# Kernel optimization log

Measured on AMD Instinct MI355X. Metric: run time of the kernel, lower is better.

The kernel has to match this reference:

```python
import jax, jax.numpy as jnp
import numpy as np


def setup_inputs() -> dict:
    key = jax.random.key(0)
    k1, k2, k3 = jax.random.split(key, 3)
    B, N, D = 16, 2048, 128
    q = jax.random.normal(k1, (B, N, D), dtype=jnp.float32)
    k = jax.random.normal(k2, (B, D, N), dtype=jnp.float32)
    v = jax.random.normal(k3, (B, N, D), dtype=jnp.float32)
    return {"q": q, "k": k, "v": v}


def reference(q, k, v):
    # scores: [B, N, N] — note NO 1/sqrt(d) scaling, matching the source
    scores = jnp.einsum('bnd,bdm->bnm', q, k)
    probs = jax.nn.softmax(scores, axis=-1)
    out = jnp.einsum('bnm,bmd->bnd', probs, v)  # [B, N, D]
    return out
```

## Files before the change

kernel.cpp:

```cpp
#include <hip/hip_runtime.h>
#include <hip/hip_bf16.h>


typedef __attribute__((ext_vector_type(8))) _Float16 f16x8;
typedef __attribute__((ext_vector_type(4))) float f32x4;

constexpr int Bz = 16;
constexpr int Nn = 2048;
constexpr int Dd = 128;
constexpr int BM = 64;
constexpr int BN = 64;

__device__ __forceinline__ int swz(int r) { return (r ^ (r >> 3)) & 7; }
__device__ __forceinline__ int swzP(int row) { return (row >> 1) & 6; }

__device__ __forceinline__ uint packh2(float a, float b) {
    union { _Float16 h[2]; uint u; } p;
    p.h[0] = (_Float16)a; p.h[1] = (_Float16)b;
    return p.u;
}
__device__ __forceinline__ ushort f2h_bits(float a) {
    union { _Float16 h; ushort u; } p;
    p.h = (_Float16)a;
    return p.u;
}

template <int CTRL>
__device__ __forceinline__ float dpp_mov(float x) {
    int y = __builtin_amdgcn_mov_dpp(__builtin_bit_cast(int, x), CTRL, 0xF, 0xF, true);
    return __builtin_bit_cast(float, y);
}
template <typename Op>
__device__ __forceinline__ float allred16(float x, Op op) {
    x = op(x, dpp_mov<0xB1>(x));
    x = op(x, dpp_mov<0x4E>(x));
    x = op(x, dpp_mov<0x124>(x));
    x = op(x, dpp_mov<0x128>(x));
    return x;
}

__global__ __launch_bounds__(256, 2)
void fattn_kernel(const float* __restrict__ qg,
                  const float* __restrict__ kg,
                  const float* __restrict__ vg,
                  float* __restrict__ og)
{
    __shared__ ushort lds_k[BN * Dd];
    __shared__ ushort lds_v[Dd * BN];
    __shared__ ushort lds_p[4][16 * BN];
    uint* const lds_k32 = (uint*)lds_k;
    uint* const lds_v32 = (uint*)lds_v;

    const int bid  = blockIdx.x;
    const int xcd  = bid & 7;
    const int idx  = bid >> 3;
    const int b    = xcd * 2 + (idx >> 5);
    const int q0   = (idx & 31) * BM;
    const int tid  = threadIdx.x;
    const int wv   = tid >> 6;
    const int lane = tid & 63;
    const int quad = lane >> 4;
    const int l15  = lane & 15;

    f16x8 qf[4];
    {
        const float* qp = qg + (size_t)(b * Nn + q0 + wv * 16 + l15) * Dd + quad * 8;
        #pragma unroll
        for (int c = 0; c < 4; ++c) {
            float4 x0 = *(const float4*)(qp + c * 32);
            float4 x1 = *(const float4*)(qp + c * 32 + 4);
            const float xv[8] = {x0.x, x0.y, x0.z, x0.w, x1.x, x1.y, x1.z, x1.w};
            union { f16x8 v; _Float16 e[8]; } u;
            #pragma unroll
            for (int j = 0; j < 8; ++j) u.e[j] = (_Float16)xv[j];
            qf[c] = u.v;
        }
    }

    f32x4 accO[8];
    #pragma unroll
    for (int i = 0; i < 8; ++i) accO[i] = f32x4{0.f, 0.f, 0.f, 0.f};
    float m_i[4], l_i[4];
    #pragma unroll
    for (int r = 0; r < 4; ++r) { m_i[r] = -1e30f; l_i[r] = 0.f; }

    const int kgrp = tid & 7;
    const int krow = tid >> 3;
    const int vgrp = tid & 15;
    const int vrow = tid >> 4;

    const float* kbase = kg + (size_t)b * Dd * Nn;
    const float* vbase = vg + (size_t)b * Nn * Dd;

    float4 kr[8], vr[8];
    auto issue_loads = [&](int n0) {
        #pragma unroll
        for (int pass = 0; pass < 2; ++pass) {
            const int d0 = krow * 2 + pass * 64;
            const float* s0 = kbase + (size_t)d0 * Nn + n0 + kgrp * 8;
            kr[pass * 4 + 0] = ((const float4*)s0)[0];
            kr[pass * 4 + 1] = ((const float4*)s0)[1];
            kr[pass * 4 + 2] = ((const float4*)(s0 + Nn))[0];
            kr[pass * 4 + 3] = ((const float4*)(s0 + Nn))[1];
            const int kk0 = vrow * 2 + pass * 32;
            const float* t0 = vbase + (size_t)(n0 + kk0) * Dd + vgrp * 8;
            vr[pass * 4 + 0] = ((const float4*)t0)[0];
            vr[pass * 4 + 1] = ((const float4*)t0)[1];
            vr[pass * 4 + 2] = ((const float4*)(t0 + Dd))[0];
            vr[pass * 4 + 3] = ((const float4*)(t0 + Dd))[1];
        }
    };
    auto write_lds = [&]() {
        #pragma unroll
        for (int pass = 0; pass < 2; ++pass) {
            const int d0 = krow * 2 + pass * 64;
            const float* av = (const float*)&kr[pass * 4 + 0];
            const float* bv = (const float*)&kr[pass * 4 + 2];
            #pragma unroll
            for (int j = 0; j < 8; ++j) {
                const int n = kgrp * 8 + j;
                lds_k32[n * (Dd / 2) + ((d0 >> 1) ^ (swz(n) << 2))] = packh2(av[j], bv[j]);
            }
            const int kk0 = vrow * 2 + pass * 32;
            const float* cv = (const float*)&vr[pass * 4 + 0];
            const float* dv = (const float*)&vr[pass * 4 + 2];
            #pragma unroll
            for (int j = 0; j < 8; ++j) {
                const int dd = vgrp * 8 + j;
                lds_v32[dd * (BN / 2) + ((kk0 >> 1) ^ (swz(dd) << 2))] = packh2(cv[j], dv[j]);
            }
        }
    };

    issue_loads(0);

    for (int it = 0; it < Nn / BN; ++it) {
        write_lds();
        __syncthreads();

        issue_loads(((it + 1) & 31) * BN);

        f32x4 accS[4];
        #pragma unroll
        for (int kt = 0; kt < 4; ++kt) {
            f32x4 s = f32x4{0.f, 0.f, 0.f, 0.f};
            const int row = kt * 16 + l15;
            const int sw = swz(row) << 3;
            #pragma unroll
            for (int c = 0; c < 4; ++c) {
                f16x8 kf = *(const f16x8*)&lds_k[row * Dd + ((c * 32 + quad * 8) ^ sw)];
                s = __builtin_amdgcn_mfma_f32_16x16x32_f16(qf[c], kf, s, 0, 0, 0);
            }
            accS[kt] = s;
        }

        float alpha[4];
        #pragma unroll
        for (int r = 0; r < 4; ++r) {
            float t = fmaxf(fmaxf(accS[0][r], accS[1][r]), fmaxf(accS[2][r], accS[3][r]));
            t = allred16(t, [](float a, float bb) { return fmaxf(a, bb); });
            const float mn = fmaxf(m_i[r], t);
            alpha[r] = __expf(m_i[r] - mn);
            m_i[r] = mn;
        }
        #pragma unroll
        for (int r = 0; r < 4; ++r) {
            float local = 0.f;
            #pragma unroll
            for (int kt = 0; kt < 4; ++kt) {
                const float p = __expf(accS[kt][r] - m_i[r]);
                accS[kt][r] = p;
                local += p;
            }
            l_i[r] = l_i[r] * alpha[r] + local;
        }

        #pragma unroll
        for (int dt = 0; dt < 8; ++dt) {
            #pragma unroll
            for (int r = 0; r < 4; ++r)
                accO[dt][r] *= alpha[r];
        }

        ushort* pl = &lds_p[wv][0];
        #pragma unroll
        for (int kt = 0; kt < 4; ++kt) {
            #pragma unroll
            for (int r = 0; r < 4; ++r) {
                const int row = quad * 4 + r;
                const int col = kt * 16 + l15;
                pl[row * BN + (col ^ (swzP(row) << 3))] = f2h_bits(accS[kt][r]);
            }
        }
        f16x8 pf[2];
        {
            const int row = l15;
            const int sw = swzP(row) << 3;
            pf[0] = *(const f16x8*)&pl[row * BN + ((quad * 8) ^ sw)];
            pf[1] = *(const f16x8*)&pl[row * BN + ((32 + quad * 8) ^ sw)];
        }

        #pragma unroll
        for (int dt = 0; dt < 8; ++dt) {
            const int row = dt * 16 + l15;
            const int sw = swz(row) << 3;
            f16x8 vf0 = *(const f16x8*)&lds_v[row * BN + ((quad * 8) ^ sw)];
            f16x8 vf1 = *(const f16x8*)&lds_v[row * BN + ((32 + quad * 8) ^ sw)];
            accO[dt] = __builtin_amdgcn_mfma_f32_16x16x32_f16(pf[0], vf0, accO[dt], 0, 0, 0);
            accO[dt] = __builtin_amdgcn_mfma_f32_16x16x32_f16(pf[1], vf1, accO[dt], 0, 0, 0);
        }
        __syncthreads();
    }

    float inv[4];
    #pragma unroll
    for (int r = 0; r < 4; ++r) {
        const float l = allred16(l_i[r], [](float a, float bb) { return a + bb; });
        inv[r] = 1.f / l;
    }
    float* ob = og + (size_t)(b * Nn + q0 + wv * 16) * Dd;
    #pragma unroll
    for (int dt = 0; dt < 8; ++dt) {
        #pragma unroll
        for (int r = 0; r < 4; ++r) {
            const int row = quad * 4 + r;
            const int col = dt * 16 + l15;
            ob[(size_t)row * Dd + col] = accO[dt][r] * inv[r];
        }
    }
}

extern "C" void kernel_launch(void* const* d_in, const int* in_sizes, int n_in,
                              void* d_out, int out_size, void* d_ws, size_t ws_size,
                              hipStream_t stream) {
    const float* q = (const float*)d_in[0];
    const float* k = (const float*)d_in[1];
    const float* v = (const float*)d_in[2];
    float* o = (float*)d_out;
    (void)d_ws; (void)ws_size; (void)in_sizes; (void)n_in; (void)out_size;
    fattn_kernel<<<dim3(Bz * (Nn / BM)), dim3(256), 0, stream>>>(q, k, v, o);
}
```

Measured before the change: 158.6 us.

## Double query tile per block so each wave handles two 16-row strips

Each block now covers 128 query rows instead of 64, and each wave processes two 16-row sub-tiles that share every K/V fragment read from LDS. This halves the global K/V traffic and fp32-to-fp16 conversion per query row, and interleaves independent MFMA chains. In exchange, register pressure roughly doubles, so launch bounds drop to one block per CU. The grid also halves to 256 blocks, which is about one wave of blocks on the device and may hurt occupancy and latency hiding.

```diff
diff --git a/kernel.cpp b/kernel.cpp
--- a/kernel.cpp
+++ b/kernel.cpp
@@ -8,11 +8,11 @@
 constexpr int Bz = 16;
 constexpr int Nn = 2048;
 constexpr int Dd = 128;
-constexpr int BM = 64;
+constexpr int BM = 128;
 constexpr int BN = 64;
 
 __device__ __forceinline__ int swz(int r) { return (r ^ (r >> 3)) & 7; }
-__device__ __forceinline__ int swzP(int row) { return (row >> 1) & 6; }
+__device__ __forceinline__ int swzP2(int row) { return ((row >> 1) & 6) | (row & 1); }
 
 __device__ __forceinline__ uint packh2(float a, float b) {
     union { _Float16 h[2]; uint u; } p;
@@ -39,7 +39,7 @@
     return x;
 }
 
-__global__ __launch_bounds__(256, 2)
+__global__ __launch_bounds__(256, 1)
 void fattn_kernel(const float* __restrict__ qg,
                   const float* __restrict__ kg,
                   const float* __restrict__ vg,
@@ -47,24 +47,25 @@
 {
     __shared__ ushort lds_k[BN * Dd];
     __shared__ ushort lds_v[Dd * BN];
-    __shared__ ushort lds_p[4][16 * BN];
+    __shared__ ushort lds_p[4][32 * BN];
     uint* const lds_k32 = (uint*)lds_k;
     uint* const lds_v32 = (uint*)lds_v;
 
     const int bid  = blockIdx.x;
     const int xcd  = bid & 7;
     const int idx  = bid >> 3;
-    const int b    = xcd * 2 + (idx >> 5);
-    const int q0   = (idx & 31) * BM;
+    const int b    = xcd * 2 + (idx >> 4);
+    const int q0   = (idx & 15) * BM;
     const int tid  = threadIdx.x;
     const int wv   = tid >> 6;
     const int lane = tid & 63;
     const int quad = lane >> 4;
     const int l15  = lane & 15;
 
-    f16x8 qf[4];
-    {
-        const float* qp = qg + (size_t)(b * Nn + q0 + wv * 16 + l15) * Dd + quad * 8;
+    f16x8 qf[2][4];
+    #pragma unroll
+    for (int s = 0; s < 2; ++s) {
+        const float* qp = qg + (size_t)(b * Nn + q0 + wv * 32 + s * 16 + l15) * Dd + quad * 8;
         #pragma unroll
         for (int c = 0; c < 4; ++c) {
             float4 x0 = *(const float4*)(qp + c * 32);
@@ -73,16 +74,19 @@
             union { f16x8 v; _Float16 e[8]; } u;
             #pragma unroll
             for (int j = 0; j < 8; ++j) u.e[j] = (_Float16)xv[j];
-            qf[c] = u.v;
-        }
-    }
-
-    f32x4 accO[8];
+            qf[s][c] = u.v;
+        }
+    }
+
+    f32x4 accO[2][8];
+    float m_i[2][4], l_i[2][4];
     #pragma unroll
-    for (int i = 0; i < 8; ++i) accO[i] = f32x4{0.f, 0.f, 0.f, 0.f};
-    float m_i[4], l_i[4];
-    #pragma unroll
-    for (int r = 0; r < 4; ++r) { m_i[r] = -1e30f; l_i[r] = 0.f; }
+    for (int s = 0; s < 2; ++s) {
+        #pragma unroll
+        for (int i = 0; i < 8; ++i) accO[s][i] = f32x4{0.f, 0.f, 0.f, 0.f};
+        #pragma unroll
+        for (int r = 0; r < 4; ++r) { m_i[s][r] = -1e30f; l_i[s][r] = 0.f; }
+    }
 
     const int kgrp = tid & 7;
     const int krow = tid >> 3;
@@ -140,64 +144,74 @@
 
         issue_loads(((it + 1) & 31) * BN);
 
-        f32x4 accS[4];
+        f32x4 accS[2][4];
         #pragma unroll
         for (int kt = 0; kt < 4; ++kt) {
-            f32x4 s = f32x4{0.f, 0.f, 0.f, 0.f};
+            f32x4 s0 = f32x4{0.f, 0.f, 0.f, 0.f};
+            f32x4 s1 = f32x4{0.f, 0.f, 0.f, 0.f};
             const int row = kt * 16 + l15;
             const int sw = swz(row) << 3;
             #pragma unroll
             for (int c = 0; c < 4; ++c) {
                 f16x8 kf = *(const f16x8*)&lds_k[row * Dd + ((c * 32 + quad * 8) ^ sw)];
-                s = __builtin_amdgcn_mfma_f32_16x16x32_f16(qf[c], kf, s, 0, 0, 0);
-            }
-            accS[kt] = s;
-        }
-
-        float alpha[4];
-        #pragma unroll
-        for (int r = 0; r < 4; ++r) {
-            float t = fmaxf(fmaxf(accS[0][r], accS[1][r]), fmaxf(accS[2][r], accS[3][r]));
-            t = allred16(t, [](float a, float bb) { return fmaxf(a, bb); });
-            const float mn = fmaxf(m_i[r], t);
-            alpha[r] = __expf(m_i[r] - mn);
-            m_i[r] = mn;
-        }
-        #pragma unroll
-        for (int r = 0; r < 4; ++r) {
-            float local = 0.f;
+                s0 = __builtin_amdgcn_mfma_f32_16x16x32_f16(qf[0][c], kf, s0, 0, 0, 0);
+                s1 = __builtin_amdgcn_mfma_f32_16x16x32_f16(qf[1][c], kf, s1, 0, 0, 0);
+            }
+            accS[0][kt] = s0;
+            accS[1][kt] = s1;
+        }
+
+        #pragma unroll
+        for (int s = 0; s < 2; ++s) {
+            float alpha[4];
+            #pragma unroll
+            for (int r = 0; r < 4; ++r) {
+                float t = fmaxf(fmaxf(accS[s][0][r], accS[s][1][r]),
+                                fmaxf(accS[s][2][r], accS[s][3][r]));
+                t = allred16(t, [](float a, float bb) { return fmaxf(a, bb); });
+                const float mn = fmaxf(m_i[s][r], t);
+                alpha[r] = __expf(m_i[s][r] - mn);
+                m_i[s][r] = mn;
+            }
+            #pragma unroll
+            for (int r = 0; r < 4; ++r) {
+                float local = 0.f;
+                #pragma unroll
+                for (int kt = 0; kt < 4; ++kt) {
+                    const float p = __expf(accS[s][kt][r] - m_i[s][r]);
+                    accS[s][kt][r] = p;
+                    local += p;
+                }
+                l_i[s][r] = l_i[s][r] * alpha[r] + local;
+            }
+            #pragma unroll
+            for (int dt = 0; dt < 8; ++dt) {
+                #pragma unroll
+                for (int r = 0; r < 4; ++r)
+                    accO[s][dt][r] *= alpha[r];
+            }
+        }
+
+        ushort* pl = &lds_p[wv][0];
+        #pragma unroll
+        for (int s = 0; s < 2; ++s) {
             #pragma unroll
             for (int kt = 0; kt < 4; ++kt) {
-                const float p = __expf(accS[kt][r] - m_i[r]);
-                accS[kt][r] = p;
-                local += p;
-            }
-            l_i[r] = l_i[r] * alpha[r] + local;
-        }
-
-        #pragma unroll
-        for (int dt = 0; dt < 8; ++dt) {
-            #pragma unroll
-            for (int r = 0; r < 4; ++r)
-                accO[dt][r] *= alpha[r];
-        }
-
-        ushort* pl = &lds_p[wv][0];
-        #pragma unroll
-        for (int kt = 0; kt < 4; ++kt) {
-            #pragma unroll
-            for (int r = 0; r < 4; ++r) {
-                const int row = quad * 4 + r;
-                const int col = kt * 16 + l15;
-                pl[row * BN + (col ^ (swzP(row) << 3))] = f2h_bits(accS[kt][r]);
-            }
-        }
-        f16x8 pf[2];
-        {
-            const int row = l15;
-            const int sw = swzP(row) << 3;
-            pf[0] = *(const f16x8*)&pl[row * BN + ((quad * 8) ^ sw)];
-            pf[1] = *(const f16x8*)&pl[row * BN + ((32 + quad * 8) ^ sw)];
+                #pragma unroll
+                for (int r = 0; r < 4; ++r) {
+                    const int lr = s * 16 + quad * 4 + r;
+                    const int col = kt * 16 + l15;
+                    pl[lr * BN + (col ^ (swzP2(lr) << 3))] = f2h_bits(accS[s][kt][r]);
+                }
+            }
+        }
+        f16x8 pf[2][2];
+        #pragma unroll
+        for (int s = 0; s < 2; ++s) {
+            const int lr = s * 16 + l15;
+            const int sw = swzP2(lr) << 3;
+            pf[s][0] = *(const f16x8*)&pl[lr * BN + ((quad * 8) ^ sw)];
+            pf[s][1] = *(const f16x8*)&pl[lr * BN + ((32 + quad * 8) ^ sw)];
         }
 
         #pragma unroll
@@ -206,26 +220,32 @@
             const int sw = swz(row) << 3;
             f16x8 vf0 = *(const f16x8*)&lds_v[row * BN + ((quad * 8) ^ sw)];
             f16x8 vf1 = *(const f16x8*)&lds_v[row * BN + ((32 + quad * 8) ^ sw)];
-            accO[dt] = __builtin_amdgcn_mfma_f32_16x16x32_f16(pf[0], vf0, accO[dt], 0, 0, 0);
-            accO[dt] = __builtin_amdgcn_mfma_f32_16x16x32_f16(pf[1], vf1, accO[dt], 0, 0, 0);
+            #pragma unroll
+            for (int s = 0; s < 2; ++s) {
+                accO[s][dt] = __builtin_amdgcn_mfma_f32_16x16x32_f16(pf[s][0], vf0, accO[s][dt], 0, 0, 0);
+                accO[s][dt] = __builtin_amdgcn_mfma_f32_16x16x32_f16(pf[s][1], vf1, accO[s][dt], 0, 0, 0);
+            }
         }
         __syncthreads();
     }
 
-    float inv[4];
     #pragma unroll
-    for (int r = 0; r < 4; ++r) {
-        const float l = allred16(l_i[r], [](float a, float bb) { return a + bb; });
-        inv[r] = 1.f / l;
-    }
-    float* ob = og + (size_t)(b * Nn + q0 + wv * 16) * Dd;
-    #pragma unroll
-    for (int dt = 0; dt < 8; ++dt) {
+    for (int s = 0; s < 2; ++s) {
+        float inv[4];
         #pragma unroll
         for (int r = 0; r < 4; ++r) {
-            const int row = quad * 4 + r;
-            const int col = dt * 16 + l15;
-            ob[(size_t)row * Dd + col] = accO[dt][r] * inv[r];
+            const float l = allred16(l_i[s][r], [](float a, float bb) { return a + bb; });
+            inv[r] = 1.f / l;
+        }
+        float* ob = og + (size_t)(b * Nn + q0 + wv * 32 + s * 16) * Dd;
+        #pragma unroll
+        for (int dt = 0; dt < 8; ++dt) {
+            #pragma unroll
+            for (int r = 0; r < 4; ++r) {
+                const int row = quad * 4 + r;
+                const int col = dt * 16 + l15;
+                ob[(size_t)row * Dd + col] = accO[s][dt][r] * inv[r];
+            }
         }
     }
 }
```

New measurement: 178.4 us. +12.5%, slower.

## Double query tile to 128 rows with 8 waves and transposed MFMA operand order

Applied to the files above, without the earlier changes.

Grows the query tile per block from 64 to 128 rows using 512 threads (8 waves), so each K/V tile staged in LDS is reused by twice as many queries and the per-thread global load work is halved. Swaps the MFMA operand order so each lane holds one query row's scores. Row max and sum then need only two cross-quad shuffles instead of per-row DPP reductions, P is written to LDS as packed uint2 stores into a padded buffer, and the output is stored as float4. The cost is fewer blocks (256), larger workgroups, and higher register pressure under launch_bounds(512,2).

```diff
diff --git a/kernel.cpp b/kernel.cpp
--- a/kernel.cpp
+++ b/kernel.cpp
@@ -8,38 +8,19 @@
 constexpr int Bz = 16;
 constexpr int Nn = 2048;
 constexpr int Dd = 128;
-constexpr int BM = 64;
+constexpr int BM = 128;
 constexpr int BN = 64;
+constexpr int PK = 72;
 
 __device__ __forceinline__ int swz(int r) { return (r ^ (r >> 3)) & 7; }
-__device__ __forceinline__ int swzP(int row) { return (row >> 1) & 6; }
 
 __device__ __forceinline__ uint packh2(float a, float b) {
     union { _Float16 h[2]; uint u; } p;
     p.h[0] = (_Float16)a; p.h[1] = (_Float16)b;
     return p.u;
 }
-__device__ __forceinline__ ushort f2h_bits(float a) {
-    union { _Float16 h; ushort u; } p;
-    p.h = (_Float16)a;
-    return p.u;
-}
-
-template <int CTRL>
-__device__ __forceinline__ float dpp_mov(float x) {
-    int y = __builtin_amdgcn_mov_dpp(__builtin_bit_cast(int, x), CTRL, 0xF, 0xF, true);
-    return __builtin_bit_cast(float, y);
-}
-template <typename Op>
-__device__ __forceinline__ float allred16(float x, Op op) {
-    x = op(x, dpp_mov<0xB1>(x));
-    x = op(x, dpp_mov<0x4E>(x));
-    x = op(x, dpp_mov<0x124>(x));
-    x = op(x, dpp_mov<0x128>(x));
-    return x;
-}
-
-__global__ __launch_bounds__(256, 2)
+
+__global__ __launch_bounds__(512, 2)
 void fattn_kernel(const float* __restrict__ qg,
                   const float* __restrict__ kg,
                   const float* __restrict__ vg,
@@ -47,15 +28,15 @@
 {
     __shared__ ushort lds_k[BN * Dd];
     __shared__ ushort lds_v[Dd * BN];
-    __shared__ ushort lds_p[4][16 * BN];
+    __shared__ ushort lds_p[8 * 16 * PK];
     uint* const lds_k32 = (uint*)lds_k;
     uint* const lds_v32 = (uint*)lds_v;
 
     const int bid  = blockIdx.x;
     const int xcd  = bid & 7;
     const int idx  = bid >> 3;
-    const int b    = xcd * 2 + (idx >> 5);
-    const int q0   = (idx & 31) * BM;
+    const int b    = xcd * 2 + (idx >> 4);
+    const int q0   = (idx & 15) * BM;
     const int tid  = threadIdx.x;
     const int wv   = tid >> 6;
     const int lane = tid & 63;
@@ -80,9 +61,7 @@
     f32x4 accO[8];
     #pragma unroll
     for (int i = 0; i < 8; ++i) accO[i] = f32x4{0.f, 0.f, 0.f, 0.f};
-    float m_i[4], l_i[4];
-    #pragma unroll
-    for (int r = 0; r < 4; ++r) { m_i[r] = -1e30f; l_i[r] = 0.f; }
+    float m_i = -1e30f, l_i = 0.f;
 
     const int kgrp = tid & 7;
     const int krow = tid >> 3;
@@ -92,43 +71,37 @@
     const float* kbase = kg + (size_t)b * Dd * Nn;
     const float* vbase = vg + (size_t)b * Nn * Dd;
 
-    float4 kr[8], vr[8];
+    float4 kr[4], vr[4];
     auto issue_loads = [&](int n0) {
-        #pragma unroll
-        for (int pass = 0; pass < 2; ++pass) {
-            const int d0 = krow * 2 + pass * 64;
-            const float* s0 = kbase + (size_t)d0 * Nn + n0 + kgrp * 8;
-            kr[pass * 4 + 0] = ((const float4*)s0)[0];
-            kr[pass * 4 + 1] = ((const float4*)s0)[1];
-            kr[pass * 4 + 2] = ((const float4*)(s0 + Nn))[0];
-            kr[pass * 4 + 3] = ((const float4*)(s0 + Nn))[1];
-            const int kk0 = vrow * 2 + pass * 32;
-            const float* t0 = vbase + (size_t)(n0 + kk0) * Dd + vgrp * 8;
-            vr[pass * 4 + 0] = ((const float4*)t0)[0];
-            vr[pass * 4 + 1] = ((const float4*)t0)[1];
-            vr[pass * 4 + 2] = ((const float4*)(t0 + Dd))[0];
-            vr[pass * 4 + 3] = ((const float4*)(t0 + Dd))[1];
-        }
+        const int d0 = krow * 2;
+        const float* s0 = kbase + (size_t)d0 * Nn + n0 + kgrp * 8;
+        kr[0] = ((const float4*)s0)[0];
+        kr[1] = ((const float4*)s0)[1];
+        kr[2] = ((const float4*)(s0 + Nn))[0];
+        kr[3] = ((const float4*)(s0 + Nn))[1];
+        const int kk0 = vrow * 2;
+        const float* t0 = vbase + (size_t)(n0 + kk0) * Dd + vgrp * 8;
+        vr[0] = ((const float4*)t0)[0];
+        vr[1] = ((const float4*)t0)[1];
+        vr[2] = ((const float4*)(t0 + Dd))[0];
+        vr[3] = ((const float4*)(t0 + Dd))[1];
     };
     auto write_lds = [&]() {
-        #pragma unroll
-        for (int pass = 0; pass < 2; ++pass) {
-            const int d0 = krow * 2 + pass * 64;
-            const float* av = (const float*)&kr[pass * 4 + 0];
-            const float* bv = (const float*)&kr[pass * 4 + 2];
-            #pragma unroll
-            for (int j = 0; j < 8; ++j) {
-                const int n = kgrp * 8 + j;
-                lds_k32[n * (Dd / 2) + ((d0 >> 1) ^ (swz(n) << 2))] = packh2(av[j], bv[j]);
-            }
-            const int kk0 = vrow * 2 + pass * 32;
-            const float* cv = (const float*)&vr[pass * 4 + 0];
-            const float* dv = (const float*)&vr[pass * 4 + 2];
-            #pragma unroll
-            for (int j = 0; j < 8; ++j) {
-                const int dd = vgrp * 8 + j;
-                lds_v32[dd * (BN / 2) + ((kk0 >> 1) ^ (swz(dd) << 2))] = packh2(cv[j], dv[j]);
-            }
+        const int d0 = krow * 2;
+        const float* av = (const float*)&kr[0];
+        const float* bv = (const float*)&kr[2];
+        #pragma unroll
+        for (int j = 0; j < 8; ++j) {
+            const int n = kgrp * 8 + j;
+            lds_k32[n * (Dd / 2) + ((d0 >> 1) ^ (swz(n) << 2))] = packh2(av[j], bv[j]);
+        }
+        const int kk0 = vrow * 2;
+        const float* cv = (const float*)&vr[0];
+        const float* dv = (const float*)&vr[2];
+        #pragma unroll
+        for (int j = 0; j < 8; ++j) {
+            const int dd = vgrp * 8 + j;
+            lds_v32[dd * (BN / 2) + ((kk0 >> 1) ^ (swz(dd) << 2))] = packh2(cv[j], dv[j]);
         }
     };
 
@@ -149,56 +122,48 @@
             #pragma unroll
             for (int c = 0; c < 4; ++c) {
                 f16x8 kf = *(const f16x8*)&lds_k[row * Dd + ((c * 32 + quad * 8) ^ sw)];
-                s = __builtin_amdgcn_mfma_f32_16x16x32_f16(qf[c], kf, s, 0, 0, 0);
+                s = __builtin_amdgcn_mfma_f32_16x16x32_f16(kf, qf[c], s, 0, 0, 0);
             }
             accS[kt] = s;
         }
 
-        float alpha[4];
-        #pragma unroll
-        for (int r = 0; r < 4; ++r) {
-            float t = fmaxf(fmaxf(accS[0][r], accS[1][r]), fmaxf(accS[2][r], accS[3][r]));
-            t = allred16(t, [](float a, float bb) { return fmaxf(a, bb); });
-            const float mn = fmaxf(m_i[r], t);
-            alpha[r] = __expf(m_i[r] - mn);
-            m_i[r] = mn;
-        }
-        #pragma unroll
-        for (int r = 0; r < 4; ++r) {
-            float local = 0.f;
-            #pragma unroll
-            for (int kt = 0; kt < 4; ++kt) {
-                const float p = __expf(accS[kt][r] - m_i[r]);
+        float mx = accS[0][0];
+        #pragma unroll
+        for (int kt = 0; kt < 4; ++kt)
+            #pragma unroll
+            for (int r = 0; r < 4; ++r)
+                mx = fmaxf(mx, accS[kt][r]);
+        mx = fmaxf(mx, __shfl_xor(mx, 16, 64));
+        mx = fmaxf(mx, __shfl_xor(mx, 32, 64));
+        const float mn = fmaxf(m_i, mx);
+        const float alpha = __expf(m_i - mn);
+        m_i = mn;
+        float local = 0.f;
+        #pragma unroll
+        for (int kt = 0; kt < 4; ++kt)
+            #pragma unroll
+            for (int r = 0; r < 4; ++r) {
+                const float p = __expf(accS[kt][r] - mn);
                 accS[kt][r] = p;
                 local += p;
             }
-            l_i[r] = l_i[r] * alpha[r] + local;
-        }
-
-        #pragma unroll
-        for (int dt = 0; dt < 8; ++dt) {
+        l_i = l_i * alpha + local;
+        #pragma unroll
+        for (int dt = 0; dt < 8; ++dt)
             #pragma unroll
             for (int r = 0; r < 4; ++r)
-                accO[dt][r] *= alpha[r];
-        }
-
-        ushort* pl = &lds_p[wv][0];
+                accO[dt][r] *= alpha;
+
+        ushort* pl = lds_p + wv * 16 * PK;
         #pragma unroll
         for (int kt = 0; kt < 4; ++kt) {
-            #pragma unroll
-            for (int r = 0; r < 4; ++r) {
-                const int row = quad * 4 + r;
-                const int col = kt * 16 + l15;
-                pl[row * BN + (col ^ (swzP(row) << 3))] = f2h_bits(accS[kt][r]);
-            }
-        }
-        f16x8 pf[2];
-        {
-            const int row = l15;
-            const int sw = swzP(row) << 3;
-            pf[0] = *(const f16x8*)&pl[row * BN + ((quad * 8) ^ sw)];
-            pf[1] = *(const f16x8*)&pl[row * BN + ((32 + quad * 8) ^ sw)];
-        }
+            uint2 w;
+            w.x = packh2(accS[kt][0], accS[kt][1]);
+            w.y = packh2(accS[kt][2], accS[kt][3]);
+            *(uint2*)(pl + l15 * PK + kt * 16 + quad * 4) = w;
+        }
+        f16x8 pf0 = *(const f16x8*)&pl[l15 * PK + quad * 8];
+        f16x8 pf1 = *(const f16x8*)&pl[l15 * PK + 32 + quad * 8];
 
         #pragma unroll
         for (int dt = 0; dt < 8; ++dt) {
@@ -206,27 +171,25 @@
             const int sw = swz(row) << 3;
             f16x8 vf0 = *(const f16x8*)&lds_v[row * BN + ((quad * 8) ^ sw)];
             f16x8 vf1 = *(const f16x8*)&lds_v[row * BN + ((32 + quad * 8) ^ sw)];
-            accO[dt] = __builtin_amdgcn_mfma_f32_16x16x32_f16(pf[0], vf0, accO[dt], 0, 0, 0);
-            accO[dt] = __builtin_amdgcn_mfma_f32_16x16x32_f16(pf[1], vf1, accO[dt], 0, 0, 0);
+            accO[dt] = __builtin_amdgcn_mfma_f32_16x16x32_f16(vf0, pf0, accO[dt], 0, 0, 0);
+            accO[dt] = __builtin_amdgcn_mfma_f32_16x16x32_f16(vf1, pf1, accO[dt], 0, 0, 0);
         }
         __syncthreads();
     }
 
-    float inv[4];
-    #pragma unroll
-    for (int r = 0; r < 4; ++r) {
-        const float l = allred16(l_i[r], [](float a, float bb) { return a + bb; });
-        inv[r] = 1.f / l;
-    }
-    float* ob = og + (size_t)(b * Nn + q0 + wv * 16) * Dd;
+    float l = l_i;
+    l += __shfl_xor(l, 16, 64);
+    l += __shfl_xor(l, 32, 64);
+    const float inv = 1.f / l;
+    float* ob = og + (size_t)(b * Nn + q0 + wv * 16 + l15) * Dd;
     #pragma unroll
     for (int dt = 0; dt < 8; ++dt) {
-        #pragma unroll
-        for (int r = 0; r < 4; ++r) {
-            const int row = quad * 4 + r;
-            const int col = dt * 16 + l15;
-            ob[(size_t)row * Dd + col] = accO[dt][r] * inv[r];
-        }
+        float4 val;
+        val.x = accO[dt][0] * inv;
+        val.y = accO[dt][1] * inv;
+        val.z = accO[dt][2] * inv;
+        val.w = accO[dt][3] * inv;
+        *(float4*)(ob + dt * 16 + quad * 4) = val;
     }
 }
 
@@ -238,5 +201,5 @@
     const float* v = (const float*)d_in[2];
     float* o = (float*)d_out;
     (void)d_ws; (void)ws_size; (void)in_sizes; (void)n_in; (void)out_size;
-    fattn_kernel<<<dim3(Bz * (Nn / BM)), dim3(256), 0, stream>>>(q, k, v, o);
+    fattn_kernel<<<dim3(Bz * (Nn / BM)), dim3(512), 0, stream>>>(q, k, v, o);
 }
```

New measurement: 150.9 us. 1.05x faster.
